# Kernel tuning notes

Measured on AMD Instinct MI355X. Metric: run time of the kernel, lower is better.

The kernel has to match this reference:

```python
import jax, jax.numpy as jnp
import numpy as np


def setup_inputs() -> dict:
    key = jax.random.key(0)
    ks = jax.random.split(key, 8)
    N, D, E, R = 300000, 64, 1000000, 100000
    all_emb = jax.random.normal(ks[0], (N, D), jnp.float32)
    # xavier-ish init for the edge MLP (Linear(2D->D), Linear(D->1))
    W1 = jax.random.normal(ks[1], (D, 2 * D), jnp.float32) / np.sqrt(2.0 * D).astype(np.float32)
    b1 = jnp.zeros((D,), jnp.float32)
    W2 = jax.random.normal(ks[2], (1, D), jnp.float32) / np.sqrt(1.0 * D).astype(np.float32)
    b2 = jnp.zeros((1,), jnp.float32)
    edge_index = jax.random.randint(ks[3], (2, E), 0, N, jnp.int32)
    rand_idx = jax.random.randint(ks[4], (2, R), 0, N, jnp.int32)
    eps_u = jax.random.uniform(ks[5], (E, 1), jnp.float32)
    rb_u = jax.random.uniform(ks[6], (E,), jnp.float32)
    return dict(all_emb=all_emb, W1=W1, b1=b1, W2=W2, b2=b2,
                edge_index=edge_index, rand_idx=rand_idx, eps_u=eps_u, rb_u=rb_u)


def reference(all_emb, W1, b1, W2, b2, edge_index, rand_idx, eps_u, rb_u):
    src, dst = edge_index[0], edge_index[1]
    # gather + concat: [E, 2D]
    edge_emb = jnp.concatenate([all_emb[src], all_emb[dst]], axis=1)
    h = jax.nn.relu(edge_emb @ W1.T + b1)            # [E, D]
    edge_logits = h @ W2.T + b2                      # [E, 1]
    # Gumbel-sigmoid gate, temperature 1.0; eps ~ U(bias, 1-bias)
    bias = 1e-4
    eps = (bias - (1.0 - bias)) * eps_u + (1.0 - bias)
    gate = jnp.log(eps) - jnp.log1p(-eps) + edge_logits
    edge_weight = jax.nn.sigmoid(gate)[:, 0]         # [E]
    # __build_prob_neighbourhood: RelaxedBernoulli(temp=0.9, probs=clamp(w,.01,.99)).rsample()
    att = jnp.clip(edge_weight, 0.01, 0.99)
    u = jnp.clip(rb_u, 1e-7, 1.0 - 1e-7)
    t = 0.9
    sample = jax.nn.sigmoid((jnp.log(att) - jnp.log1p(-att) + jnp.log(u) - jnp.log1p(-u)) / t)
    mask = jax.lax.stop_gradient((sample > 0.0).astype(sample.dtype))
    mat = sample * mask
    # sparse rebuild: (edge_index, mat) + graph_random (rand_idx, 0.05), then coalesce
    rand_vals = jnp.full((rand_idx.shape[1],), 0.05, mat.dtype)
    rows = jnp.concatenate([src, rand_idx[0]])
    cols = jnp.concatenate([dst, rand_idx[1]])
    vals = jnp.concatenate([mat, rand_vals])
    order = jnp.lexsort((cols, rows))                # sort by (row, col)
    rows_s, cols_s, vals_s = rows[order], cols[order], vals[order]
    change = jnp.concatenate([jnp.ones((1,), bool),
                              (rows_s[1:] != rows_s[:-1]) | (cols_s[1:] != cols_s[:-1])])
    seg = jnp.cumsum(change) - 1                     # run id per sorted entry
    sums = jax.ops.segment_sum(vals_s, seg, num_segments=vals.shape[0])
    # coalesced value placed at first occurrence of each unique (row,col); dups zeroed
    out_vals = jnp.where(change, sums[seg], 0.0)
    return rows_s, cols_s, out_vals
```

## Files before the change

kernel.cpp:

```cpp
#include <hip/hip_runtime.h>
#include <stdint.h>

typedef unsigned short u16;
typedef unsigned int   u32;
typedef __attribute__((ext_vector_type(8))) short bf16x8;
typedef __attribute__((ext_vector_type(4))) float f32x4;

#define RSTRIDE 32

__device__ __forceinline__ float bflo(u32 u){ return __uint_as_float(u << 16); }
__device__ __forceinline__ u32 f2bf(float f){
  u32 u = __float_as_uint(f);
  return (u + 0x7fffu + ((u >> 16) & 1u)) >> 16;
}
__device__ __forceinline__ float qbf(float f){ return __uint_as_float(f2bf(f) << 16); }

__global__ void k_zero(int* __restrict__ c, int N){
  int i = blockIdx.x * 256 + threadIdx.x;
  if (i < N) c[i] = 0;
}

__global__ void __launch_bounds__(256) k_mlp_fused(
    const u16* __restrict__ emb, const u16* __restrict__ W1,
    const u16* __restrict__ b1, const u16* __restrict__ W2,
    const u16* __restrict__ b2,
    const int* __restrict__ src, const int* __restrict__ dst,
    const u16* __restrict__ eps_u, const u16* __restrict__ rb_u,
    const int* __restrict__ rand0, const int* __restrict__ rand1,
    int* __restrict__ cnt, u32* __restrict__ packed,
    int E, int R, int ntp)
{
  int lane = threadIdx.x & 63;
  int c    = lane & 15;
  int quad = lane >> 4;
  int wid  = blockIdx.x * 4 + (threadIdx.x >> 6);
  int wstride = gridDim.x * 4;

  {
    int gtid = blockIdx.x * 256 + threadIdx.x;
    int gsz  = gridDim.x * 256;
    for (int i = gtid; i < R; i += gsz){
      int row = rand0[i];
      int rk = atomicAdd(&cnt[row], 1);
      if (rk < RSTRIDE)
        packed[(size_t)row * RSTRIDE + rk] = ((u32)rand1[i] << 13) | 7501u;
    }
  }

  bf16x8 bfr[4][4];
  #pragma unroll
  for (int ks = 0; ks < 4; ks++)
    #pragma unroll
    for (int t = 0; t < 4; t++)
      bfr[ks][t] = *(const bf16x8*)(W1 + (size_t)(t*16 + c)*128 + ks*32 + quad*8);

  float b1v[4], w2v[4];
  #pragma unroll
  for (int t = 0; t < 4; t++){
    b1v[t] = bflo((u32)b1[t*16 + c]);
    w2v[t] = bflo((u32)W2[t*16 + c]);
  }
  float b2v = bflo((u32)b2[0]);

  int nd = 0;
  if (wid < ntp){
    int idx = wid * 32 + (lane & 31);
    if (idx >= E) idx = E - 1;
    nd = (lane < 32) ? src[idx] : dst[idx];
  }

  for (int tp = wid; tp < ntp; tp += wstride){
    int e_base = tp * 32;

    int tpn = tp + wstride;
    int ndn = 0;
    if (tpn < ntp){
      int idxn = tpn * 32 + (lane & 31);
      if (idxn >= E) idxn = E - 1;
      ndn = (lane < 32) ? src[idxn] : dst[idxn];
    }

    int s0 = __shfl(nd, c),      d0 = __shfl(nd, 32 + c);
    int s1 = __shfl(nd, 16 + c), d1 = __shfl(nd, 48 + c);

    int tile = c >> 2, r = c & 3;
    int eo32 = tile * 16 + quad * 4 + r;
    int e_o  = e_base + eo32;
    bool act = (c < 8) && (e_o < E);
    int s_e = __shfl(nd, eo32);
    int d_e = __shfl(nd, 32 + eo32);

    int rk = 0;
    if (act) rk = atomicAdd(&cnt[s_e], 1);

    bf16x8 a0[4], a1[4];
    #pragma unroll
    for (int ks = 0; ks < 4; ks++){
      a0[ks] = *(const bf16x8*)(emb + (size_t)(ks < 2 ? s0 : d0) * 64 + (ks & 1) * 32 + quad * 8);
      a1[ks] = *(const bf16x8*)(emb + (size_t)(ks < 2 ? s1 : d1) * 64 + (ks & 1) * 32 + quad * 8);
    }

    float ue = 0.f, uu_raw = 0.f;
    if (act){
      ue     = bflo((u32)eps_u[e_o]);
      uu_raw = bflo((u32)rb_u[e_o]);
    }

    f32x4 acc0[4], acc1[4];
    #pragma unroll
    for (int t = 0; t < 4; t++){
      acc0[t] = (f32x4){0.f,0.f,0.f,0.f};
      acc1[t] = (f32x4){0.f,0.f,0.f,0.f};
    }
    #pragma unroll
    for (int ks = 0; ks < 4; ks++){
      #pragma unroll
      for (int t = 0; t < 4; t++){
        acc0[t] = __builtin_amdgcn_mfma_f32_16x16x32_bf16(a0[ks], bfr[ks][t], acc0[t], 0, 0, 0);
        acc1[t] = __builtin_amdgcn_mfma_f32_16x16x32_bf16(a1[ks], bfr[ks][t], acc1[t], 0, 0, 0);
      }
    }

    float pr0[4], pr1[4];
    #pragma unroll
    for (int rr = 0; rr < 4; rr++){
      float h0 = fmaxf(acc0[0][rr] + b1v[0], 0.f);
      float h1 = fmaxf(acc0[1][rr] + b1v[1], 0.f);
      float h2 = fmaxf(acc0[2][rr] + b1v[2], 0.f);
      float h3 = fmaxf(acc0[3][rr] + b1v[3], 0.f);
      pr0[rr] = h0*w2v[0] + h1*w2v[1] + h2*w2v[2] + h3*w2v[3];
      float g0 = fmaxf(acc1[0][rr] + b1v[0], 0.f);
      float g1 = fmaxf(acc1[1][rr] + b1v[1], 0.f);
      float g2 = fmaxf(acc1[2][rr] + b1v[2], 0.f);
      float g3 = fmaxf(acc1[3][rr] + b1v[3], 0.f);
      pr1[rr] = g0*w2v[0] + g1*w2v[1] + g2*w2v[2] + g3*w2v[3];
    }
    #pragma unroll
    for (int d = 1; d < 16; d <<= 1){
      #pragma unroll
      for (int rr = 0; rr < 4; rr++){
        pr0[rr] += __shfl_xor(pr0[rr], d);
        pr1[rr] += __shfl_xor(pr1[rr], d);
      }
    }

    if (act){
      float pv0 = (r==0)?pr0[0]:(r==1)?pr0[1]:(r==2)?pr0[2]:pr0[3];
      float pv1 = (r==0)?pr1[0]:(r==1)?pr1[1]:(r==2)?pr1[2]:pr1[3];
      float logit = (tile ? pv1 : pv0) + b2v;
      float eps = fmaf(-0.9998f, ue, 0.9999f);
      float gate = (__log2f(eps) - __log2f(1.0f - eps)) * 0.69314718f + logit;
      gate = fminf(fmaxf(gate, -4.59511985f), 4.59511985f);
      float uu = fminf(fmaxf(uu_raw, 1e-7f), 1.0f - 1e-7f);
      float lu = (__log2f(uu) - __log2f(1.0f - uu)) * 0.69314718f;
      float l  = (gate + lu) * (1.0f / 0.9f);
      float ee = __builtin_amdgcn_exp2f(-l * 1.44269504f);
      float val = 1.0f / (1.0f + ee);
      u32 h = f2bf(val);
      u32 code = (h >= 8192u) ? (h - 8192u) : 0u;
      if (rk < RSTRIDE)
        packed[(size_t)s_e * RSTRIDE + rk] = ((u32)d_e << 13) | code;
    }

    nd = ndn;
  }
}

__global__ void k_scan1(const int* __restrict__ cnt, int* __restrict__ rowstart,
                        int* __restrict__ bsum, int N){
  __shared__ int sh[256];
  int blk = blockIdx.x, tid = threadIdx.x;
  int base = blk * 1024 + tid * 4;
  int v0 = (base + 0 < N) ? min(cnt[base + 0], RSTRIDE) : 0;
  int v1 = (base + 1 < N) ? min(cnt[base + 1], RSTRIDE) : 0;
  int v2 = (base + 2 < N) ? min(cnt[base + 2], RSTRIDE) : 0;
  int v3 = (base + 3 < N) ? min(cnt[base + 3], RSTRIDE) : 0;
  int tot = v0 + v1 + v2 + v3;
  sh[tid] = tot;
  __syncthreads();
  for (int off = 1; off < 256; off <<= 1){
    int t2 = (tid >= off) ? sh[tid - off] : 0;
    __syncthreads();
    sh[tid] += t2;
    __syncthreads();
  }
  int excl = sh[tid] - tot;
  if (base + 0 < N) rowstart[base + 0] = excl;
  if (base + 1 < N) rowstart[base + 1] = excl + v0;
  if (base + 2 < N) rowstart[base + 2] = excl + v0 + v1;
  if (base + 3 < N) rowstart[base + 3] = excl + v0 + v1 + v2;
  if (tid == 255) bsum[blk] = sh[255];
}

__global__ void k_scan2(const int* __restrict__ bsum, int* __restrict__ boff, int NB){
  __shared__ int sh[512];
  int tid = threadIdx.x;
  int v = (tid < NB) ? bsum[tid] : 0;
  sh[tid] = v;
  __syncthreads();
  for (int off = 1; off < 512; off <<= 1){
    int t2 = (tid >= off) ? sh[tid - off] : 0;
    __syncthreads();
    sh[tid] += t2;
    __syncthreads();
  }
  boff[tid] = sh[tid] - v;
}

__global__ void k_scan3(int* __restrict__ rowstart, const int* __restrict__ boff, int N){
  int add = boff[blockIdx.x];
  int base = blockIdx.x * 1024 + threadIdx.x * 4;
  #pragma unroll
  for (int q = 0; q < 4; q++)
    if (base + q < N) rowstart[base + q] += add;
}

__global__ void k_emit(const int* __restrict__ rowstart, const int* __restrict__ cnt,
                       u32* __restrict__ packed, float* __restrict__ out,
                       int N, int M){
  int r = blockIdx.x * 256 + threadIdx.x;
  if (r >= N) return;
  int deg = min(cnt[r], RSTRIDE);
  u32* seg = packed + (size_t)r * RSTRIDE;
  for (int i = 1; i < deg; i++){
    u32 p = seg[i];
    int j = i - 1;
    while (j >= 0 && seg[j] > p){ seg[j+1] = seg[j]; j--; }
    seg[j+1] = p;
  }
  int b = rowstart[r];
  float rf = qbf((float)r);
  int i = 0;
  while (i < deg){
    u32 p = seg[i];
    u32 col = p >> 13;
    u32 lo  = p & 8191u;
    float sum = __uint_as_float((lo ? lo + 8192u : 0u) << 16);
    int j = i + 1;
    while (j < deg && (seg[j] >> 13) == col){
      u32 l2 = seg[j] & 8191u;
      sum += __uint_as_float((l2 ? l2 + 8192u : 0u) << 16);
      j++;
    }
    float cf = qbf((float)col);
    out[b + i] = rf; out[M + b + i] = cf; out[2 * M + b + i] = qbf(sum);
    for (int q = i + 1; q < j; q++){
      out[b + q] = rf; out[M + b + q] = cf; out[2 * M + b + q] = 0.f;
    }
    i = j;
  }
}

extern "C" void kernel_launch(void* const* d_in, const int* in_sizes, int n_in,
                              void* d_out, int out_size, void* d_ws, size_t ws_size,
                              hipStream_t stream){
  (void)n_in; (void)out_size; (void)ws_size;
  const u16* all_emb = (const u16*)d_in[0];
  const u16* W1   = (const u16*)d_in[1];
  const u16* b1   = (const u16*)d_in[2];
  const u16* W2   = (const u16*)d_in[3];
  const u16* b2   = (const u16*)d_in[4];
  const int* edge_index = (const int*)d_in[5];
  const int* rand_idx   = (const int*)d_in[6];
  const u16* eps_u = (const u16*)d_in[7];
  const u16* rb_u  = (const u16*)d_in[8];

  int N = in_sizes[0] / 64;
  int E = in_sizes[5] / 2;
  int R = in_sizes[6] / 2;
  int M = E + R;
  const int* src   = edge_index;
  const int* dst   = edge_index + E;
  const int* rand0 = rand_idx;
  const int* rand1 = rand_idx + R;

  int* cnt      = (int*)d_ws;
  int* rowstart = cnt + N;
  int* bsum     = rowstart + N;
  int* boff     = bsum + 512;
  u32* packed   = (u32*)(boff + 512);

  k_zero<<<(N + 255) / 256, 256, 0, stream>>>(cnt, N);
  int ntp = (E + 31) / 32;
  k_mlp_fused<<<2048, 256, 0, stream>>>(all_emb, W1, b1, W2, b2, src, dst,
                                        eps_u, rb_u, rand0, rand1,
                                        cnt, packed, E, R, ntp);
  int NB = (N + 1023) / 1024;
  k_scan1<<<NB, 256, 0, stream>>>(cnt, rowstart, bsum, N);
  k_scan2<<<1, 512, 0, stream>>>(bsum, boff, NB);
  k_scan3<<<NB, 256, 0, stream>>>(rowstart, boff, N);
  k_emit<<<(N + 255) / 256, 256, 0, stream>>>(rowstart, cnt, packed,
                                              (float*)d_out, N, M);
}
```

Baseline: 269.6 us.

## Fold scan block-offset add into emit and sort short rows in registers

Removes the k_scan3 launch by having k_emit add the per-block offset itself. For rows with at most 16 entries, k_emit loads the packed segment with vector loads into registers, sorts it with a fixed 16-element sorting network, and coalesces duplicate columns without touching global memory again. Rows with more than 16 entries still use the in-memory insertion sort. The network costs a fixed amount of compare-swap work even for very short rows, and the fully unrolled duplicate scan may raise register pressure.

Measured after the change: 239.3 us. 11.2% less time.

```diff
diff --git a/kernel.cpp b/kernel.cpp
--- a/kernel.cpp
+++ b/kernel.cpp
@@ -14,6 +14,10 @@
   return (u + 0x7fffu + ((u >> 16) & 1u)) >> 16;
 }
 __device__ __forceinline__ float qbf(float f){ return __uint_as_float(f2bf(f) << 16); }
+__device__ __forceinline__ float decp(u32 p){
+  u32 lo = p & 8191u;
+  return __uint_as_float((lo ? lo + 8192u : 0u) << 16);
+}
 
 __global__ void k_zero(int* __restrict__ c, int N){
   int i = blockIdx.x * 256 + threadIdx.x;
@@ -207,20 +211,61 @@
   boff[tid] = sh[tid] - v;
 }
 
-__global__ void k_scan3(int* __restrict__ rowstart, const int* __restrict__ boff, int N){
-  int add = boff[blockIdx.x];
-  int base = blockIdx.x * 1024 + threadIdx.x * 4;
-  #pragma unroll
-  for (int q = 0; q < 4; q++)
-    if (base + q < N) rowstart[base + q] += add;
-}
-
-__global__ void k_emit(const int* __restrict__ rowstart, const int* __restrict__ cnt,
-                       u32* __restrict__ packed, float* __restrict__ out,
-                       int N, int M){
+#define CAS(a,b) { u32 x = v[a], y = v[b]; v[a] = min(x,y); v[b] = max(x,y); }
+
+__global__ void __launch_bounds__(256) k_emit(
+    const int* __restrict__ rowstart, const int* __restrict__ boff,
+    const int* __restrict__ cnt, u32* __restrict__ packed,
+    float* __restrict__ out, int N, int M){
   int r = blockIdx.x * 256 + threadIdx.x;
   if (r >= N) return;
   int deg = min(cnt[r], RSTRIDE);
+  int b = rowstart[r] + boff[r >> 10];
+  float rf = qbf((float)r);
+
+  if (deg <= 16){
+    const uint4* seg4 = (const uint4*)(packed + (size_t)r * RSTRIDE);
+    uint4 q0 = seg4[0], q1 = seg4[1], q2 = seg4[2], q3 = seg4[3];
+    u32 v[16];
+    v[0]=q0.x; v[1]=q0.y; v[2]=q0.z; v[3]=q0.w;
+    v[4]=q1.x; v[5]=q1.y; v[6]=q1.z; v[7]=q1.w;
+    v[8]=q2.x; v[9]=q2.y; v[10]=q2.z; v[11]=q2.w;
+    v[12]=q3.x; v[13]=q3.y; v[14]=q3.z; v[15]=q3.w;
+    #pragma unroll
+    for (int i = 0; i < 16; i++) if (i >= deg) v[i] = 0xFFFFFFFFu;
+
+    CAS(0,1) CAS(2,3) CAS(4,5) CAS(6,7) CAS(8,9) CAS(10,11) CAS(12,13) CAS(14,15)
+    CAS(0,2) CAS(1,3) CAS(4,6) CAS(5,7) CAS(8,10) CAS(9,11) CAS(12,14) CAS(13,15)
+    CAS(1,2) CAS(5,6) CAS(9,10) CAS(13,14)
+    CAS(0,4) CAS(1,5) CAS(2,6) CAS(3,7) CAS(8,12) CAS(9,13) CAS(10,14) CAS(11,15)
+    CAS(2,4) CAS(3,5) CAS(10,12) CAS(11,13)
+    CAS(1,2) CAS(3,4) CAS(5,6) CAS(9,10) CAS(11,12) CAS(13,14)
+    CAS(0,8) CAS(1,9) CAS(2,10) CAS(3,11) CAS(4,12) CAS(5,13) CAS(6,14) CAS(7,15)
+    CAS(4,8) CAS(5,9) CAS(6,10) CAS(7,11)
+    CAS(2,4) CAS(3,5) CAS(6,8) CAS(7,9) CAS(10,12) CAS(11,13)
+    CAS(1,2) CAS(3,4) CAS(5,6) CAS(7,8) CAS(9,10) CAS(11,12) CAS(13,14)
+
+    #pragma unroll
+    for (int i = 0; i < 16; i++){
+      if (i < deg){
+        u32 coli = v[i] >> 13;
+        bool head = (i == 0) || ((v[i-1] >> 13) != coli);
+        float s = decp(v[i]);
+        bool run = true;
+        #pragma unroll
+        for (int j = i + 1; j < 16; j++){
+          run = run && (j < deg) && ((v[j] >> 13) == coli);
+          if (run) s += decp(v[j]);
+        }
+        float cf = qbf((float)coli);
+        out[b + i]         = rf;
+        out[M + b + i]     = cf;
+        out[2 * M + b + i] = head ? qbf(s) : 0.f;
+      }
+    }
+    return;
+  }
+
   u32* seg = packed + (size_t)r * RSTRIDE;
   for (int i = 1; i < deg; i++){
     u32 p = seg[i];
@@ -228,18 +273,14 @@
     while (j >= 0 && seg[j] > p){ seg[j+1] = seg[j]; j--; }
     seg[j+1] = p;
   }
-  int b = rowstart[r];
-  float rf = qbf((float)r);
   int i = 0;
   while (i < deg){
     u32 p = seg[i];
     u32 col = p >> 13;
-    u32 lo  = p & 8191u;
-    float sum = __uint_as_float((lo ? lo + 8192u : 0u) << 16);
+    float sum = decp(p);
     int j = i + 1;
     while (j < deg && (seg[j] >> 13) == col){
-      u32 l2 = seg[j] & 8191u;
-      sum += __uint_as_float((l2 ? l2 + 8192u : 0u) << 16);
+      sum += decp(seg[j]);
       j++;
     }
     float cf = qbf((float)col);
@@ -288,7 +329,6 @@
   int NB = (N + 1023) / 1024;
   k_scan1<<<NB, 256, 0, stream>>>(cnt, rowstart, bsum, N);
   k_scan2<<<1, 512, 0, stream>>>(bsum, boff, NB);
-  k_scan3<<<NB, 256, 0, stream>>>(rowstart, boff, N);
-  k_emit<<<(N + 255) / 256, 256, 0, stream>>>(rowstart, cnt, packed,
+  k_emit<<<(N + 255) / 256, 256, 0, stream>>>(rowstart, boff, cnt, packed,
                                               (float*)d_out, N, M);
 }
```
